# Optimization experiments

Hardware: AMD Instinct MI355X
Metric: run time of the kernel (lower is better)

## Reference

```python
import jax, jax.numpy as jnp
import numpy as np

B, S, C, HEADS = 1, 4096, 640, 8
AH, AW = 64, 64            # attn-resolution grid, AH*AW == S
MH, MW = 512, 512          # full-res mask size
NEG = -1e9                 # finite large negative (safe for fully-masked rows)


def nearest_resize(x, h, w):
    # torch F.interpolate(mode='nearest'): idx = floor(i * H_in / H_out)
    H, W = x.shape[-2], x.shape[-1]
    ri = (jnp.arange(h) * H) // h
    ci = (jnp.arange(w) * W) // w
    return x[..., ri, :][..., :, ci]


def sdpa(q, k, v, mask, heads):
    # q,k,v: [B,S,C]; mask: [B,1,S,S] bool (True = attend), broadcasts over heads
    b, s, c = q.shape
    d = c // heads
    qh = q.reshape(b, s, heads, d).transpose(0, 2, 1, 3)  # bhsd
    kh = k.reshape(b, s, heads, d).transpose(0, 2, 1, 3)
    vh = v.reshape(b, s, heads, d).transpose(0, 2, 1, 3)
    scores = jnp.einsum('bhqd,bhkd->bhqk', qh, kh) / jnp.sqrt(jnp.asarray(d, qh.dtype))
    scores = jnp.where(mask, scores, NEG)
    attn = jax.nn.softmax(scores, axis=-1)
    out = jnp.einsum('bhqk,bhkd->bhqd', attn, vh)
    return out.transpose(0, 2, 1, 3).reshape(b, s, c)


def setup_inputs():
    key = jax.random.key(0)
    ks = jax.random.split(key, 14)
    std = 1.0 / np.sqrt(C)
    w = lambda k: (jax.random.normal(k, (C, C), jnp.float32) * std)
    return {
        'hidden_states': jax.random.normal(ks[0], (B, S, C), jnp.float32),
        'mask': jax.random.randint(ks[1], (B, 1, MH, MW), 0, 4, jnp.int32),
        'inpainting_mask': jax.random.randint(ks[2], (B, 1, MH, MW), 0, 2, jnp.int32),
        'Wq': w(ks[3]), 'Wk': w(ks[4]), 'Wv': w(ks[5]),
        'Wq_ent': w(ks[6]), 'Wk_ent': w(ks[7]), 'Wv_ent': w(ks[8]),
        'Wq_out': w(ks[9]), 'Wk_out': w(ks[10]), 'Wv_out': w(ks[11]),
        'Wo': w(ks[12]),
    }


def reference(hidden_states, mask, inpainting_mask, Wq, Wk, Wv,
              Wq_ent, Wk_ent, Wv_ent, Wq_out, Wk_out, Wv_out, Wo):
    residual = hidden_states
    b, s, c = hidden_states.shape

    # --- interpolation-derived masks (kept as [B,1,S,S]; broadcasts over heads) ---
    m = nearest_resize(mask, AH, AW).reshape(b, 1, s)                 # entity labels
    attn_mask = m[:, :, :, None] == m[:, :, None, :]                  # same-entity [B,1,S,S]
    im = nearest_resize(inpainting_mask, AH, AW).reshape(b, 1, s)
    outside_key = (im[:, :, None, :] == 0)                            # [B,1,1,S]
    attn_mask_outside = attn_mask & outside_key                       # [B,1,S,S]

    # --- projections ---
    q = hidden_states @ Wq.T
    k = hidden_states @ Wk.T
    v = hidden_states @ Wv.T
    q_e = hidden_states @ Wq_ent.T
    k_e = hidden_states @ Wk_ent.T
    v_e = hidden_states @ Wv_ent.T
    q_o = hidden_states @ Wq_out.T
    k_o = hidden_states @ Wk_out.T
    v_o = hidden_states @ Wv_out.T

    # --- three SDPA branches ---
    hs_orig = sdpa(q, k, v, attn_mask, HEADS)            # original attention
    hs_ent = sdpa(q_e, k_e, v_e, attn_mask, 1)           # entity attention (1 head)
    hs_out = sdpa(q_o, k_o, v_o, attn_mask_outside, HEADS)  # outside attention

    hs = hs_orig + hs_ent + hs_out
    return hs @ Wo.T + residual
```

## Files before the change

### kernel.cpp

```cpp
#include <hip/hip_runtime.h>
#include <cstdint>

typedef __attribute__((ext_vector_type(8))) short bf16x8;
typedef __attribute__((ext_vector_type(4))) short bf16x4;
typedef __attribute__((ext_vector_type(4))) float f32x4;

#define S_LEN 4096
#define CDIM  640
#define NPROJ 5760

__device__ __forceinline__ f32x4 mfma16(bf16x4 a, bf16x4 b, f32x4 c){
#if defined(__HIP_DEVICE_COMPILE__) && __HIP_DEVICE_COMPILE__
  return __builtin_amdgcn_mfma_f32_16x16x16bf16_1k(a, b, c, 0, 0, 0);
#else
  (void)a; (void)b;
  return c;
#endif
}

__device__ __forceinline__ void gload_lds(const unsigned short* g, unsigned short* l){
#if defined(__HIP_DEVICE_COMPILE__) && __HIP_DEVICE_COMPILE__
  __builtin_amdgcn_global_load_lds((const __attribute__((address_space(1))) unsigned int*)g,
                                   (__attribute__((address_space(3))) unsigned int*)l, 16, 0, 0);
#else
  (void)g; (void)l;
#endif
}

__device__ __forceinline__ unsigned short f2bf(float f){
  union { float f; uint32_t u; } v; v.f = f;
  uint32_t u = v.u;
  return (unsigned short)((u + 0x7fffu + ((u >> 16) & 1u)) >> 16);
}
__device__ __forceinline__ float b2f(unsigned short h){
  union { uint32_t u; float f; } v; v.u = ((uint32_t)h) << 16;
  return v.f;
}

__global__ void k_labels(const int* __restrict__ mask, const int* __restrict__ inp,
                         int* __restrict__ labels){
  int s = blockIdx.x * 256 + threadIdx.x;
  if (s >= S_LEN) return;
  int y = s >> 6, x = s & 63;
  int off = (y * 8) * 512 + x * 8;
  int m = mask[off] & 0xff;
  int o = (inp[off] == 0) ? 0x100 : 0;
  labels[s] = m | o;
}

__global__ void k_hist(const int* __restrict__ labels, int* __restrict__ boff, int* __restrict__ cnt){
  __shared__ int h[4];
  if (threadIdx.x < 4) h[threadIdx.x] = 0;
  __syncthreads();
  for (int s = threadIdx.x; s < S_LEN; s += 256) atomicAdd(&h[labels[s] & 3], 1);
  __syncthreads();
  if (threadIdx.x == 0){
    int a = 0;
    for (int c = 0; c < 4; c++){ boff[c] = a; a += h[c]; }
    boff[4] = a;
  }
  if (threadIdx.x < 4) cnt[threadIdx.x] = 0;
}

__global__ void k_perm(const int* __restrict__ labels, const int* __restrict__ boff,
                       int* __restrict__ cnt, int* __restrict__ perm,
                       int* __restrict__ inv, int* __restrict__ labP){
  int s = blockIdx.x * 256 + threadIdx.x;
  if (s >= S_LEN) return;
  int lab = labels[s];
  int c = lab & 3;
  int pos = boff[c] + atomicAdd(&cnt[c], 1);
  perm[pos] = s; inv[s] = pos; labP[pos] = lab;
}

__global__ void k_tiles(const int* __restrict__ labP, const int* __restrict__ boff,
                        int4* __restrict__ qtinfo, float* __restrict__ rowsum){
  int t = threadIdx.x;
  __shared__ int nkt[32];
  if (t < 32){
    int c0 = labP[t * 128] & 3, c1 = labP[t * 128 + 127] & 3;
    int lo = boff[c0] & ~127, hi = (boff[c1 + 1] + 127) & ~127;
    qtinfo[t].x = lo; qtinfo[t].y = hi; qtinfo[t].w = 0;
    nkt[t] = (hi - lo) >> 7;
  }
  __syncthreads();
  if (t == 0){
    int a = 0;
    for (int i = 0; i < 32; i++){ qtinfo[i].z = a; a += nkt[i]; }
  }
  for (int s = t; s < S_LEN; s += 256) rowsum[s] = 0.f;
}

__global__ void k_cvt_hs(const float* __restrict__ src, unsigned short* __restrict__ dst, int n){
  int idx = (blockIdx.x * 256 + threadIdx.x) * 4;
  if (idx >= n) return;
  float4 v = *(const float4*)(src + idx);
  ushort4 o;
  o.x = f2bf(v.x); o.y = f2bf(v.y); o.z = f2bf(v.z); o.w = f2bf(v.w);
  *(ushort4*)(dst + idx) = o;
}

struct WPtrs { const float* w[10]; };

__global__ void k_cvt_w(WPtrs p, unsigned short* __restrict__ dst){
  int e = (blockIdx.x * 256 + threadIdx.x) * 4;
  if (e >= 10 * 409600) return;
  int a = e / 409600, r = e % 409600;
  float sc = (a == 0 || a == 6) ? 0.11180339887498948f
           : (a == 3 ? 0.03952847075210474f : 1.0f);
  float4 v = *(const float4*)(p.w[a] + r);
  ushort4 o;
  o.x = f2bf(v.x * sc); o.y = f2bf(v.y * sc); o.z = f2bf(v.z * sc); o.w = f2bf(v.w * sc);
  *(ushort4*)(dst + e) = o;
}

template<int EPI>
__global__ __launch_bounds__(256) void k_gemm(const unsigned short* __restrict__ A,
                                              const unsigned short* __restrict__ B,
                                              int M, int N, int K, int ldc,
                                              const int* __restrict__ rowmap,
                                              unsigned short* __restrict__ Cb,
                                              float* __restrict__ Cf,
                                              const float* __restrict__ resid){
  __shared__ __align__(16) unsigned short As[128 * 64];
  __shared__ __align__(16) unsigned short Bs[128 * 64];
  int m0 = blockIdx.y * 128, n0 = blockIdx.x * 128;
  int tid = threadIdx.x;
  int wid = tid >> 6, lane = tid & 63;
  int quad = lane >> 4, l16 = lane & 15;
  int wm = (wid >> 1) * 64, wn = (wid & 1) * 64;
  f32x4 acc[4][4];
#pragma unroll
  for (int i = 0; i < 4; i++)
#pragma unroll
    for (int j = 0; j < 4; j++) acc[i][j] = f32x4{0.f, 0.f, 0.f, 0.f};

  for (int k0 = 0; k0 < K; k0 += 64){
    __syncthreads();
#pragma unroll
    for (int u = 0; u < 4; u++){
      int c = tid + u * 256;
      int row = c >> 3, off = (c & 7) * 8;
      gload_lds(&A[(size_t)(m0 + row) * K + k0 + off], &As[c * 8]);
      gload_lds(&B[(size_t)(n0 + row) * K + k0 + off], &Bs[c * 8]);
    }
    __syncthreads();
#pragma unroll
    for (int ks = 0; ks < 2; ks++){
      bf16x8 af[4], bfr[4];
#pragma unroll
      for (int t = 0; t < 4; t++){
        af[t]  = *(const bf16x8*)(&As[(wm + t * 16 + l16) * 64 + ks * 32 + quad * 8]);
        bfr[t] = *(const bf16x8*)(&Bs[(wn + t * 16 + l16) * 64 + ks * 32 + quad * 8]);
      }
#pragma unroll
      for (int mt = 0; mt < 4; mt++)
#pragma unroll
        for (int nt = 0; nt < 4; nt++)
          acc[mt][nt] = __builtin_amdgcn_mfma_f32_16x16x32_bf16(af[mt], bfr[nt], acc[mt][nt], 0, 0, 0);
    }
  }
#pragma unroll
  for (int mt = 0; mt < 4; mt++)
#pragma unroll
    for (int nt = 0; nt < 4; nt++)
#pragma unroll
      for (int r = 0; r < 4; r++){
        int row = m0 + wm + mt * 16 + quad * 4 + r;
        int col = n0 + wn + nt * 16 + l16;
        float v = acc[mt][nt][r];
        if (EPI == 0){
          Cb[(size_t)rowmap[row] * ldc + col] = f2bf(v);
        } else {
          int ro = rowmap[row];
          Cf[(size_t)ro * ldc + col] = v + resid[(size_t)ro * ldc + col];
        }
      }
}

__global__ void k_transpose_v(const unsigned short* __restrict__ proj, unsigned short* __restrict__ vT){
  __shared__ unsigned short T[64][65];
  int z = blockIdx.z;
  int s0 = blockIdx.x * 64, c0 = blockIdx.y * 64;
  int colbase = 1280 + z * 1920 + c0;
  unsigned short* dst = vT + (size_t)z * CDIM * S_LEN;
  int tid = threadIdx.x;
  for (int i = tid; i < 64 * 64; i += 256){
    int r = i >> 6, c = i & 63;
    T[r][c] = proj[(size_t)(s0 + r) * NPROJ + colbase + c];
  }
  __syncthreads();
  for (int i = tid; i < 64 * 64; i += 256){
    int c = i >> 6, r = i & 63;
    dst[(size_t)(c0 + c) * S_LEN + s0 + r] = T[r][c];
  }
}

#define KP 84
#define VP 76
__global__ __launch_bounds__(256, 2) void k_attn80(const unsigned short* __restrict__ proj,
                                                   const unsigned short* __restrict__ vT,
                                                   const int* __restrict__ labP,
                                                   const int4* __restrict__ qtinfo,
                                                   unsigned short* __restrict__ opart,
                                                   float* __restrict__ lpP){
  __shared__ __align__(16) unsigned short Ks[2][64 * KP];
  __shared__ __align__(16) unsigned short Vt[2][80 * VP];
  __shared__ __align__(16) int labk[2][64];
  int tid = threadIdx.x, wid = tid >> 6, lane = tid & 63;
  int quad = lane >> 4, l16 = lane & 15;
  int qt = blockIdx.x >> 1, half = blockIdx.x & 1;
  int q0 = qt * 128;
  int h  = blockIdx.y;
  bool OUTSIDE = (blockIdx.z == 1);
  int qc = (OUTSIDE ? 3840 : 0) + h * 80;
  int kc = (OUTSIDE ? 4480 : 640) + h * 80;
  const unsigned short* vTb = vT + (size_t)(OUTSIDE ? 2 : 0) * CDIM * S_LEN;
  int4 qi = qtinfo[qt];
  int t0 = qi.x >> 6, t1 = qi.y >> 6;
  int nt = t1 - t0;
  int mid = t0 + ((nt + 1) >> 1);
  int ta = half ? mid : t0;
  int tb = half ? t1 : mid;

  int qrow0 = q0 + wid * 32 + l16;
  int qrow1 = qrow0 + 16;
  bf16x4 qf0[5], qf1[5];
#pragma unroll
  for (int dc = 0; dc < 5; dc++){
    qf0[dc] = *(const bf16x4*)&proj[(size_t)qrow0 * NPROJ + qc + dc * 16 + quad * 4];
    qf1[dc] = *(const bf16x4*)&proj[(size_t)qrow1 * NPROJ + qc + dc * 16 + quad * 4];
  }
  int lq0 = labP[qrow0] & 0xff, lq1 = labP[qrow1] & 0xff;

  float lp0 = 0.f, lp1 = 0.f;
  f32x4 Oc0[5], Oc1[5];
#pragma unroll
  for (int t = 0; t < 5; t++){ Oc0[t] = f32x4{0.f,0.f,0.f,0.f}; Oc1[t] = f32x4{0.f,0.f,0.f,0.f}; }

  const int cS0 = tid, cS1 = tid + 256, cS2 = tid + 512, cS3 = tid + 768, cS4 = tid + 1024;
  const int kga0 = (cS0 / 20) * NPROJ + kc + (cS0 % 20) * 4;
  const int kga1 = (cS1 / 20) * NPROJ + kc + (cS1 % 20) * 4;
  const int kga2 = (cS2 / 20) * NPROJ + kc + (cS2 % 20) * 4;
  const int kga3 = (cS3 / 20) * NPROJ + kc + (cS3 % 20) * 4;
  const int kga4 = (cS4 / 20) * NPROJ + kc + (cS4 % 20) * 4;
  const int kls0 = (cS0 / 20) * KP + (cS0 % 20) * 4;
  const int kls1 = (cS1 / 20) * KP + (cS1 % 20) * 4;
  const int kls2 = (cS2 / 20) * KP + (cS2 % 20) * 4;
  const int kls3 = (cS3 / 20) * KP + (cS3 % 20) * 4;
  const int kls4 = (cS4 / 20) * KP + (cS4 % 20) * 4;
  const int vga0 = (h * 80 + (cS0 >> 4)) * S_LEN + (cS0 & 15) * 4;
  const int vga1 = (h * 80 + (cS1 >> 4)) * S_LEN + (cS1 & 15) * 4;
  const int vga2 = (h * 80 + (cS2 >> 4)) * S_LEN + (cS2 & 15) * 4;
  const int vga3 = (h * 80 + (cS3 >> 4)) * S_LEN + (cS3 & 15) * 4;
  const int vga4 = (h * 80 + (cS4 >> 4)) * S_LEN + (cS4 & 15) * 4;
  const int vls0 = (cS0 >> 4) * VP + (cS0 & 15) * 4;
  const int vls1 = (cS1 >> 4) * VP + (cS1 & 15) * 4;
  const int vls2 = (cS2 >> 4) * VP + (cS2 & 15) * 4;
  const int vls3 = (cS3 >> 4) * VP + (cS3 & 15) * 4;
  const int vls4 = (cS4 >> 4) * VP + (cS4 & 15) * 4;

  uint2 kr0, kr1, kr2, kr3, kr4, vr0, vr1, vr2, vr3, vr4;
  int lreg = 0;

#define LOADT(kt_) do {                                              \
    int _k0 = (kt_) * 64;                                            \
    size_t _kb = (size_t)_k0 * NPROJ;                                \
    kr0 = *(const uint2*)&proj[_kb + kga0];                          \
    kr1 = *(const uint2*)&proj[_kb + kga1];                          \
    kr2 = *(const uint2*)&proj[_kb + kga2];                          \
    kr3 = *(const uint2*)&proj[_kb + kga3];                          \
    kr4 = *(const uint2*)&proj[_kb + kga4];                          \
    vr0 = *(const uint2*)&vTb[(size_t)(vga0 + _k0)];                 \
    vr1 = *(const uint2*)&vTb[(size_t)(vga1 + _k0)];                 \
    vr2 = *(const uint2*)&vTb[(size_t)(vga2 + _k0)];                 \
    vr3 = *(const uint2*)&vTb[(size_t)(vga3 + _k0)];                 \
    vr4 = *(const uint2*)&vTb[(size_t)(vga4 + _k0)];                 \
    if (tid < 64) lreg = labP[_k0 + tid];                            \
  } while (0)

#define WRITET(b) do {                                               \
    *(uint2*)&Ks[b][kls0] = kr0;                                     \
    *(uint2*)&Ks[b][kls1] = kr1;                                     \
    *(uint2*)&Ks[b][kls2] = kr2;                                     \
    *(uint2*)&Ks[b][kls3] = kr3;                                     \
    *(uint2*)&Ks[b][kls4] = kr4;                                     \
    *(uint2*)&Vt[b][vls0] = vr0;                                     \
    *(uint2*)&Vt[b][vls1] = vr1;                                     \
    *(uint2*)&Vt[b][vls2] = vr2;                                     \
    *(uint2*)&Vt[b][vls3] = vr3;                                     \
    *(uint2*)&Vt[b][vls4] = vr4;                                     \
    if (tid < 64) labk[b][tid] = lreg;                               \
  } while (0)

  LOADT(ta);
  WRITET(0);
  if (ta + 1 < tb) LOADT(ta + 1);
  __syncthreads();

  int cur = 0;
  for (int kt = ta; kt < tb; kt++){
    int nxt = cur ^ 1;
    if (kt + 1 < tb){
      WRITET(nxt);
      if (kt + 2 < tb) LOADT(kt + 2);
    }

#pragma unroll
    for (int kg = 0; kg < 4; kg++){
      f32x4 sa0 = f32x4{0.f,0.f,0.f,0.f}, sa1 = f32x4{0.f,0.f,0.f,0.f};
#pragma unroll
      for (int dc = 0; dc < 5; dc++){
        bf16x4 kf = *(const bf16x4*)&Ks[cur][(kg * 16 + l16) * KP + dc * 16 + quad * 4];
        sa0 = mfma16(kf, qf0[dc], sa0);
        sa1 = mfma16(kf, qf1[dc], sa1);
      }
      int4 lk4 = *(const int4*)&labk[cur][kg * 16 + quad * 4];
      bool m0 = !OUTSIDE || (lk4.x & 0x100), m1 = !OUTSIDE || (lk4.y & 0x100);
      bool m2 = !OUTSIDE || (lk4.z & 0x100), m3 = !OUTSIDE || (lk4.w & 0x100);
      int k0l = lk4.x & 0xff, k1l = lk4.y & 0xff, k2l = lk4.z & 0xff, k3l = lk4.w & 0xff;
      bf16x4 pf0, pf1;
      {
        float p0 = (k0l == lq0 && m0) ? __expf(sa0[0]) : 0.f;
        float p1 = (k1l == lq0 && m1) ? __expf(sa0[1]) : 0.f;
        float p2 = (k2l == lq0 && m2) ? __expf(sa0[2]) : 0.f;
        float p3 = (k3l == lq0 && m3) ? __expf(sa0[3]) : 0.f;
        lp0 += (p0 + p1) + (p2 + p3);
        pf0[0] = (short)f2bf(p0); pf0[1] = (short)f2bf(p1);
        pf0[2] = (short)f2bf(p2); pf0[3] = (short)f2bf(p3);
      }
      {
        float p0 = (k0l == lq1 && m0) ? __expf(sa1[0]) : 0.f;
        float p1 = (k1l == lq1 && m1) ? __expf(sa1[1]) : 0.f;
        float p2 = (k2l == lq1 && m2) ? __expf(sa1[2]) : 0.f;
        float p3 = (k3l == lq1 && m3) ? __expf(sa1[3]) : 0.f;
        lp1 += (p0 + p1) + (p2 + p3);
        pf1[0] = (short)f2bf(p0); pf1[1] = (short)f2bf(p1);
        pf1[2] = (short)f2bf(p2); pf1[3] = (short)f2bf(p3);
      }
#pragma unroll
      for (int dt = 0; dt < 5; dt++){
        bf16x4 vf = *(const bf16x4*)&Vt[cur][(dt * 16 + l16) * VP + kg * 16 + quad * 4];
        Oc0[dt] = mfma16(vf, pf0, Oc0[dt]);
        Oc1[dt] = mfma16(vf, pf1, Oc1[dt]);
      }
    }
    __syncthreads();
    cur = nxt;
  }
#undef LOADT
#undef WRITET
  lp0 += __shfl_xor(lp0, 16); lp0 += __shfl_xor(lp0, 32);
  lp1 += __shfl_xor(lp1, 16); lp1 += __shfl_xor(lp1, 32);
  int hz = half * 2 + (int)blockIdx.z;
  if (quad == 0){
    lpP[(size_t)(hz * 8 + h) * S_LEN + qrow0] = lp0;
    lpP[(size_t)(hz * 8 + h) * S_LEN + qrow1] = lp1;
  }
  unsigned short* dst = opart + (size_t)hz * S_LEN * CDIM;
#pragma unroll
  for (int dt = 0; dt < 5; dt++){
    ushort4 o;
    o.x = f2bf(Oc0[dt][0]); o.y = f2bf(Oc0[dt][1]);
    o.z = f2bf(Oc0[dt][2]); o.w = f2bf(Oc0[dt][3]);
    *(ushort4*)&dst[(size_t)qrow0 * CDIM + h * 80 + dt * 16 + quad * 4] = o;
    o.x = f2bf(Oc1[dt][0]); o.y = f2bf(Oc1[dt][1]);
    o.z = f2bf(Oc1[dt][2]); o.w = f2bf(Oc1[dt][3]);
    *(ushort4*)&dst[(size_t)qrow1 * CDIM + h * 80 + dt * 16 + quad * 4] = o;
  }
}

__global__ __launch_bounds__(256) void k_comb(const unsigned short* __restrict__ opart,
                                              const float* __restrict__ lpP,
                                              unsigned short* __restrict__ planes){
  int i = blockIdx.x * 256 + threadIdx.x;
  int z = blockIdx.y;
  int qrow = i / 160, c4 = (i % 160) * 4;
  int h = c4 / 80;
  size_t o0 = ((size_t)(z)     * S_LEN + qrow) * CDIM + c4;
  size_t o1 = ((size_t)(2 + z) * S_LEN + qrow) * CDIM + c4;
  float lp = lpP[(size_t)(z * 8 + h) * S_LEN + qrow]
           + lpP[(size_t)((2 + z) * 8 + h) * S_LEN + qrow];
  float iL = 1.f / lp;
  ushort4 a = *(const ushort4*)&opart[o0];
  ushort4 b = *(const ushort4*)&opart[o1];
  ushort4 o;
  o.x = f2bf((b2f(a.x) + b2f(b.x)) * iL);
  o.y = f2bf((b2f(a.y) + b2f(b.y)) * iL);
  o.z = f2bf((b2f(a.z) + b2f(b.z)) * iL);
  o.w = f2bf((b2f(a.w) + b2f(b.w)) * iL);
  *(ushort4*)&planes[(size_t)z * S_LEN * CDIM + (size_t)qrow * CDIM + c4] = o;
}

__global__ __launch_bounds__(256) void k_ent_qk(const unsigned short* __restrict__ proj,
                                                const int* __restrict__ labP,
                                                const int4* __restrict__ qtinfo,
                                                unsigned short* __restrict__ Sbuf,
                                                float* __restrict__ rowsum){
  int qt = blockIdx.y;
  int4 qi = qtinfo[qt];
  int nkt = (qi.y - qi.x) >> 7;
  if ((int)blockIdx.x >= nkt) return;
  int m0 = qt * 128, n0 = qi.x + blockIdx.x * 128;
  __shared__ __align__(16) unsigned short As[128 * 64];
  __shared__ __align__(16) unsigned short Bs[128 * 64];
  __shared__ int lQ[128], lK[128];
  int tid = threadIdx.x, wid = tid >> 6, lane = tid & 63;
  int quad = lane >> 4, l16 = lane & 15;
  int wm = (wid >> 1) * 64, wn = (wid & 1) * 64;
  if (tid < 128) lQ[tid] = labP[m0 + tid] & 0xff;
  else           lK[tid - 128] = labP[n0 + tid - 128] & 0xff;
  f32x4 acc[4][4];
#pragma unroll
  for (int i = 0; i < 4; i++)
#pragma unroll
    for (int j = 0; j < 4; j++) acc[i][j] = f32x4{0.f, 0.f, 0.f, 0.f};

  for (int k0 = 0; k0 < 640; k0 += 64){
    __syncthreads();
#pragma unroll
    for (int u = 0; u < 4; u++){
      int c = tid + u * 256;
      int row = c >> 3, off = (c & 7) * 8;
      gload_lds(&proj[(size_t)(m0 + row) * NPROJ + 1920 + k0 + off], &As[c * 8]);
      gload_lds(&proj[(size_t)(n0 + row) * NPROJ + 2560 + k0 + off], &Bs[c * 8]);
    }
    __syncthreads();
#pragma unroll
    for (int ks = 0; ks < 2; ks++){
      bf16x8 af[4], bfr[4];
#pragma unroll
      for (int t = 0; t < 4; t++){
        af[t]  = *(const bf16x8*)(&As[(wm + t * 16 + l16) * 64 + ks * 32 + quad * 8]);
        bfr[t] = *(const bf16x8*)(&Bs[(wn + t * 16 + l16) * 64 + ks * 32 + quad * 8]);
      }
#pragma unroll
      for (int mt = 0; mt < 4; mt++)
#pragma unroll
        for (int nt = 0; nt < 4; nt++)
          acc[mt][nt] = __builtin_amdgcn_mfma_f32_16x16x32_bf16(af[mt], bfr[nt], acc[mt][nt], 0, 0, 0);
    }
  }
  unsigned short* St = Sbuf + ((size_t)(qi.z + blockIdx.x)) * 16384;
#pragma unroll
  for (int mt = 0; mt < 4; mt++)
#pragma unroll
    for (int r = 0; r < 4; r++){
      int lrow = wm + mt * 16 + quad * 4 + r;
      int myq = lQ[lrow];
      float psum = 0.f;
#pragma unroll
      for (int nt = 0; nt < 4; nt++){
        int lcol = wn + nt * 16 + l16;
        float p = (myq == lK[lcol]) ? __expf(acc[mt][nt][r]) : 0.f;
        St[lrow * 128 + lcol] = f2bf(p);
        psum += p;
      }
#pragma unroll
      for (int m = 1; m < 16; m <<= 1) psum += __shfl_xor(psum, m);
      if (l16 == 0) atomicAdd(&rowsum[m0 + lrow], psum);
    }
}

__global__ __launch_bounds__(256) void k_ent_pv(const unsigned short* __restrict__ Sbuf,
                                                const unsigned short* __restrict__ veT,
                                                const int4* __restrict__ qtinfo,
                                                const float* __restrict__ rowsum,
                                                const unsigned short* __restrict__ planes,
                                                unsigned short* __restrict__ attnS){
  int qt = blockIdx.y, d0 = blockIdx.x * 128;
  int4 qi = qtinfo[qt];
  int m0 = qt * 128;
  int nk = qi.y - qi.x;
  __shared__ __align__(16) unsigned short As[128 * 32];
  __shared__ __align__(16) unsigned short Bs[128 * 32];
  int tid = threadIdx.x, wid = tid >> 6, lane = tid & 63;
  int quad = lane >> 4, l16 = lane & 15;
  int wm = (wid >> 1) * 64, wn = (wid & 1) * 64;
  f32x4 acc[4][4];
#pragma unroll
  for (int i = 0; i < 4; i++)
#pragma unroll
    for (int j = 0; j < 4; j++) acc[i][j] = f32x4{0.f, 0.f, 0.f, 0.f};

  for (int kk = 0; kk < nk; kk += 32){
    const unsigned short* St = Sbuf + ((size_t)(qi.z + (kk >> 7))) * 16384;
    int kloc = kk & 127;
    __syncthreads();
#pragma unroll
    for (int u = 0; u < 2; u++){
      int c = tid + u * 256;
      int row = c >> 2, off = (c & 3) * 8;
      gload_lds(&St[row * 128 + kloc + off], &As[c * 8]);
      gload_lds(&veT[(size_t)(d0 + row) * S_LEN + qi.x + kk + off], &Bs[c * 8]);
    }
    __syncthreads();
    bf16x8 af[4], bfr[4];
#pragma unroll
    for (int t = 0; t < 4; t++){
      af[t]  = *(const bf16x8*)(&As[(wm + t * 16 + l16) * 32 + quad * 8]);
      bfr[t] = *(const bf16x8*)(&Bs[(wn + t * 16 + l16) * 32 + quad * 8]);
    }
#pragma unroll
    for (int mt = 0; mt < 4; mt++)
#pragma unroll
      for (int nt = 0; nt < 4; nt++)
        acc[mt][nt] = __builtin_amdgcn_mfma_f32_16x16x32_bf16(af[mt], bfr[nt], acc[mt][nt], 0, 0, 0);
  }
#pragma unroll
  for (int mt = 0; mt < 4; mt++)
#pragma unroll
    for (int r = 0; r < 4; r++){
      int row = m0 + wm + mt * 16 + quad * 4 + r;
      float invL = 1.f / rowsum[row];
#pragma unroll
      for (int nt = 0; nt < 4; nt++){
        int col = d0 + wn + nt * 16 + l16;
        size_t idx = (size_t)row * CDIM + col;
        float v = acc[mt][nt][r] * invL + b2f(planes[idx]) + b2f(planes[(size_t)S_LEN * CDIM + idx]);
        attnS[idx] = f2bf(v);
      }
    }
}

extern "C" void kernel_launch(void* const* d_in, const int* in_sizes, int n_in,
                              void* d_out, int out_size, void* d_ws, size_t ws_size,
                              hipStream_t stream){
  const float* hs  = (const float*)d_in[0];
  const int* mask  = (const int*)d_in[1];
  const int* inp   = (const int*)d_in[2];
  char* ws = (char*)d_ws;
  int*            labels  = (int*)(ws + 0);
  int*            boff    = (int*)(ws + 16384);
  int*            cnt     = (int*)(ws + 16640);
  int*            perm    = (int*)(ws + 16896);
  int*            inv     = (int*)(ws + 33280);
  int*            labP    = (int*)(ws + 49664);
  int4*           qtinfo  = (int4*)(ws + 66560);
  float*          rowsum  = (float*)(ws + 67072);
  unsigned short* hsb     = (unsigned short*)(ws + 131072);
  unsigned short* Wall    = (unsigned short*)(ws + 5373952);
  unsigned short* proj    = (unsigned short*)(ws + 13565952);
  unsigned short* vT      = (unsigned short*)(ws + 60751872);
  unsigned short* planes  = (unsigned short*)(ws + 76480512);
  unsigned short* Sbuf    = (unsigned short*)(ws + 86966272);
  unsigned short* attnS   = (unsigned short*)(ws + 120520704);
  unsigned short* Wob     = Wall + 9 * 409600;
  unsigned short* opart   = Sbuf;
  float*          lpP     = (float*)(ws + 86966272 + 20971520);

  k_labels<<<16, 256, 0, stream>>>(mask, inp, labels);
  k_hist<<<1, 256, 0, stream>>>(labels, boff, cnt);
  k_perm<<<16, 256, 0, stream>>>(labels, boff, cnt, perm, inv, labP);
  k_tiles<<<1, 256, 0, stream>>>(labP, boff, qtinfo, rowsum);
  k_cvt_hs<<<(S_LEN * CDIM / 4 + 255) / 256, 256, 0, stream>>>(hs, hsb, S_LEN * CDIM);
  WPtrs wp;
  for (int i = 0; i < 10; i++) wp.w[i] = (const float*)d_in[3 + i];
  k_cvt_w<<<(10 * 409600 / 4 + 255) / 256, 256, 0, stream>>>(wp, Wall);

  k_gemm<0><<<dim3(45, 32), 256, 0, stream>>>(hsb, Wall, S_LEN, NPROJ, CDIM, NPROJ,
                                              inv, proj, nullptr, nullptr);
  k_transpose_v<<<dim3(64, 10, 3), 256, 0, stream>>>(proj, vT);

  k_attn80<<<dim3(64, 8, 2), 256, 0, stream>>>(proj, vT, labP, qtinfo, opart, lpP);
  k_comb<<<dim3(2560, 2), 256, 0, stream>>>(opart, lpP, planes);

  k_ent_qk<<<dim3(32, 32), 256, 0, stream>>>(proj, labP, qtinfo, Sbuf, rowsum);
  k_ent_pv<<<dim3(5, 32), 256, 0, stream>>>(Sbuf, vT + (size_t)1 * CDIM * S_LEN,
                                            qtinfo, rowsum, planes, attnS);

  k_gemm<1><<<dim3(5, 32), 256, 0, stream>>>(attnS, Wob, S_LEN, CDIM, CDIM, CDIM,
                                             perm, nullptr, (float*)d_out, hs);
}
```

Measured before the change: 411.7 us.

## Double attention query tile to 256 rows with 512-thread blocks sharing K/V tiles

The 8-head attention kernel now processes 256 query rows per block using 512 threads instead of 128 rows with 256 threads. Each K/V tile loaded into LDS is reused by twice as many query rows, and the load work is split so half the threads fetch K and half fetch V, which cuts per-thread address registers. The key-tile range becomes the union of two query tiles' ranges, so blocks may scan extra masked keys. The grid is halved, which lowers block count and may reduce occupancy or load balance.

```diff
diff --git a/kernel.cpp b/kernel.cpp
--- a/kernel.cpp
+++ b/kernel.cpp
@@ -198,7 +198,7 @@
 
 #define KP 84
 #define VP 76
-__global__ __launch_bounds__(256, 2) void k_attn80(const unsigned short* __restrict__ proj,
+__global__ __launch_bounds__(512, 4) void k_attn80(const unsigned short* __restrict__ proj,
                                                    const unsigned short* __restrict__ vT,
                                                    const int* __restrict__ labP,
                                                    const int4* __restrict__ qtinfo,
@@ -210,14 +210,15 @@
   int tid = threadIdx.x, wid = tid >> 6, lane = tid & 63;
   int quad = lane >> 4, l16 = lane & 15;
   int qt = blockIdx.x >> 1, half = blockIdx.x & 1;
-  int q0 = qt * 128;
+  int q0 = qt * 256;
   int h  = blockIdx.y;
   bool OUTSIDE = (blockIdx.z == 1);
   int qc = (OUTSIDE ? 3840 : 0) + h * 80;
   int kc = (OUTSIDE ? 4480 : 640) + h * 80;
   const unsigned short* vTb = vT + (size_t)(OUTSIDE ? 2 : 0) * CDIM * S_LEN;
-  int4 qi = qtinfo[qt];
-  int t0 = qi.x >> 6, t1 = qi.y >> 6;
+  int4 qa = qtinfo[qt * 2], qb = qtinfo[qt * 2 + 1];
+  int lo = min(qa.x, qb.x), hi = max(qa.y, qb.y);
+  int t0 = lo >> 6, t1 = hi >> 6;
   int nt = t1 - t0;
   int mid = t0 + ((nt + 1) >> 1);
   int ta = half ? mid : t0;
@@ -238,58 +239,58 @@
 #pragma unroll
   for (int t = 0; t < 5; t++){ Oc0[t] = f32x4{0.f,0.f,0.f,0.f}; Oc1[t] = f32x4{0.f,0.f,0.f,0.f}; }
 
-  const int cS0 = tid, cS1 = tid + 256, cS2 = tid + 512, cS3 = tid + 768, cS4 = tid + 1024;
-  const int kga0 = (cS0 / 20) * NPROJ + kc + (cS0 % 20) * 4;
-  const int kga1 = (cS1 / 20) * NPROJ + kc + (cS1 % 20) * 4;
-  const int kga2 = (cS2 / 20) * NPROJ + kc + (cS2 % 20) * 4;
-  const int kga3 = (cS3 / 20) * NPROJ + kc + (cS3 % 20) * 4;
-  const int kga4 = (cS4 / 20) * NPROJ + kc + (cS4 % 20) * 4;
-  const int kls0 = (cS0 / 20) * KP + (cS0 % 20) * 4;
-  const int kls1 = (cS1 / 20) * KP + (cS1 % 20) * 4;
-  const int kls2 = (cS2 / 20) * KP + (cS2 % 20) * 4;
-  const int kls3 = (cS3 / 20) * KP + (cS3 % 20) * 4;
-  const int kls4 = (cS4 / 20) * KP + (cS4 % 20) * 4;
-  const int vga0 = (h * 80 + (cS0 >> 4)) * S_LEN + (cS0 & 15) * 4;
-  const int vga1 = (h * 80 + (cS1 >> 4)) * S_LEN + (cS1 & 15) * 4;
-  const int vga2 = (h * 80 + (cS2 >> 4)) * S_LEN + (cS2 & 15) * 4;
-  const int vga3 = (h * 80 + (cS3 >> 4)) * S_LEN + (cS3 & 15) * 4;
-  const int vga4 = (h * 80 + (cS4 >> 4)) * S_LEN + (cS4 & 15) * 4;
-  const int vls0 = (cS0 >> 4) * VP + (cS0 & 15) * 4;
-  const int vls1 = (cS1 >> 4) * VP + (cS1 & 15) * 4;
-  const int vls2 = (cS2 >> 4) * VP + (cS2 & 15) * 4;
-  const int vls3 = (cS3 >> 4) * VP + (cS3 & 15) * 4;
-  const int vls4 = (cS4 >> 4) * VP + (cS4 & 15) * 4;
-
-  uint2 kr0, kr1, kr2, kr3, kr4, vr0, vr1, vr2, vr3, vr4;
+  const bool ISK = (tid < 256);
+  const int t5 = ISK ? tid : (tid - 256);
+  const unsigned short* gb = ISK ? proj : vTb;
+  const int km = ISK ? NPROJ : 1;
+  int ga0, ga1, ga2, ga3, ga4, ls0, ls1, ls2, ls3, ls4;
+  {
+    const int c0_ = t5, c1_ = t5 + 256, c2_ = t5 + 512, c3_ = t5 + 768, c4_ = t5 + 1024;
+    if (ISK){
+      ga0 = (c0_ / 20) * NPROJ + kc + (c0_ % 20) * 4;
+      ga1 = (c1_ / 20) * NPROJ + kc + (c1_ % 20) * 4;
+      ga2 = (c2_ / 20) * NPROJ + kc + (c2_ % 20) * 4;
+      ga3 = (c3_ / 20) * NPROJ + kc + (c3_ % 20) * 4;
+      ga4 = (c4_ / 20) * NPROJ + kc + (c4_ % 20) * 4;
+      ls0 = (c0_ / 20) * KP + (c0_ % 20) * 4;
+      ls1 = (c1_ / 20) * KP + (c1_ % 20) * 4;
+      ls2 = (c2_ / 20) * KP + (c2_ % 20) * 4;
+      ls3 = (c3_ / 20) * KP + (c3_ % 20) * 4;
+      ls4 = (c4_ / 20) * KP + (c4_ % 20) * 4;
+    } else {
+      ga0 = (h * 80 + (c0_ >> 4)) * S_LEN + (c0_ & 15) * 4;
+      ga1 = (h * 80 + (c1_ >> 4)) * S_LEN + (c1_ & 15) * 4;
+      ga2 = (h * 80 + (c2_ >> 4)) * S_LEN + (c2_ & 15) * 4;
+      ga3 = (h * 80 + (c3_ >> 4)) * S_LEN + (c3_ & 15) * 4;
+      ga4 = (h * 80 + (c4_ >> 4)) * S_LEN + (c4_ & 15) * 4;
+      ls0 = (c0_ >> 4) * VP + (c0_ & 15) * 4;
+      ls1 = (c1_ >> 4) * VP + (c1_ & 15) * 4;
+      ls2 = (c2_ >> 4) * VP + (c2_ & 15) * 4;
+      ls3 = (c3_ >> 4) * VP + (c3_ & 15) * 4;
+      ls4 = (c4_ >> 4) * VP + (c4_ & 15) * 4;
+    }
+  }
+
+  uint2 r0, r1, r2, r3, r4;
   int lreg = 0;
 
 #define LOADT(kt_) do {                                              \
-    int _k0 = (kt_) * 64;                                            \
-    size_t _kb = (size_t)_k0 * NPROJ;                                \
-    kr0 = *(const uint2*)&proj[_kb + kga0];                          \
-    kr1 = *(const uint2*)&proj[_kb + kga1];                          \
-    kr2 = *(const uint2*)&proj[_kb + kga2];                          \
-    kr3 = *(const uint2*)&proj[_kb + kga3];                          \
-    kr4 = *(const uint2*)&proj[_kb + kga4];                          \
-    vr0 = *(const uint2*)&vTb[(size_t)(vga0 + _k0)];                 \
-    vr1 = *(const uint2*)&vTb[(size_t)(vga1 + _k0)];                 \
-    vr2 = *(const uint2*)&vTb[(size_t)(vga2 + _k0)];                 \
-    vr3 = *(const uint2*)&vTb[(size_t)(vga3 + _k0)];                 \
-    vr4 = *(const uint2*)&vTb[(size_t)(vga4 + _k0)];                 \
-    if (tid < 64) lreg = labP[_k0 + tid];                            \
+    size_t _ob = (size_t)((kt_) * 64) * (size_t)km;                  \
+    r0 = *(const uint2*)&gb[_ob + ga0];                              \
+    r1 = *(const uint2*)&gb[_ob + ga1];                              \
+    r2 = *(const uint2*)&gb[_ob + ga2];                              \
+    r3 = *(const uint2*)&gb[_ob + ga3];                              \
+    r4 = *(const uint2*)&gb[_ob + ga4];                              \
+    if (tid < 64) lreg = labP[(kt_) * 64 + tid];                     \
   } while (0)
 
 #define WRITET(b) do {                                               \
-    *(uint2*)&Ks[b][kls0] = kr0;                                     \
-    *(uint2*)&Ks[b][kls1] = kr1;                                     \
-    *(uint2*)&Ks[b][kls2] = kr2;                                     \
-    *(uint2*)&Ks[b][kls3] = kr3;                                     \
-    *(uint2*)&Ks[b][kls4] = kr4;                                     \
-    *(uint2*)&Vt[b][vls0] = vr0;                                     \
-    *(uint2*)&Vt[b][vls1] = vr1;                                     \
-    *(uint2*)&Vt[b][vls2] = vr2;                                     \
-    *(uint2*)&Vt[b][vls3] = vr3;                                     \
-    *(uint2*)&Vt[b][vls4] = vr4;                                     \
+    unsigned short* _lb = ISK ? Ks[b] : Vt[b];                       \
+    *(uint2*)&_lb[ls0] = r0;                                         \
+    *(uint2*)&_lb[ls1] = r1;                                         \
+    *(uint2*)&_lb[ls2] = r2;                                         \
+    *(uint2*)&_lb[ls3] = r3;                                         \
+    *(uint2*)&_lb[ls4] = r4;                                         \
     if (tid < 64) labk[b][tid] = lreg;                               \
   } while (0)
 
@@ -562,7 +563,7 @@
                                               inv, proj, nullptr, nullptr);
   k_transpose_v<<<dim3(64, 10, 3), 256, 0, stream>>>(proj, vT);
 
-  k_attn80<<<dim3(64, 8, 2), 256, 0, stream>>>(proj, vT, labP, qtinfo, opart, lpP);
+  k_attn80<<<dim3(32, 8, 2), 512, 0, stream>>>(proj, vT, labP, qtinfo, opart, lpP);
   k_comb<<<dim3(2560, 2), 256, 0, stream>>>(opart, lpP, planes);
 
   k_ent_qk<<<dim3(32, 32), 256, 0, stream>>>(proj, labP, qtinfo, Sbuf, rowsum);
```

After: 537.4 us. 30.5% more time.
